# Kernel optimization log

Hardware: AMD Instinct MI355X
Metric: run time of the kernel (lower is better)

Reference implementation:

```python
import jax, jax.numpy as jnp
import numpy as np

N = 50000
E = 800000
FEAT = 128
HID = 128
HEADS = 8
HEAD_DIM = HID // HEADS  # 16
NEG_SLOPE = 0.2


def _gat_layer(x, W, a_src, a_dst, b, src, dst, num_nodes):
    # x: [N, Fin]; W: [Fin, H*C]; a_src/a_dst: [H, C]; b: [H*C]
    H, C = a_src.shape
    h = (x @ W).reshape(num_nodes, H, C)               # [N,H,C]
    alpha_s = jnp.einsum('nhc,hc->nh', h, a_src)       # [N,H]
    alpha_d = jnp.einsum('nhc,hc->nh', h, a_dst)       # [N,H]
    e = jax.nn.leaky_relu(alpha_s[src] + alpha_d[dst], NEG_SLOPE)  # [E,H]
    # segment softmax over destination nodes (every node has a self-loop)
    m = jax.ops.segment_max(e, dst, num_segments=num_nodes)
    e = jnp.exp(e - m[dst])
    s = jax.ops.segment_sum(e, dst, num_segments=num_nodes)
    alpha = e / (s[dst] + 1e-16)                       # [E,H]
    msg = alpha[:, :, None] * h[src]                   # [E,H,C]
    out = jax.ops.segment_sum(msg, dst, num_segments=num_nodes)
    return out.reshape(num_nodes, H * C) + b


def setup_inputs() -> dict:
    key = jax.random.key(0)
    ks = jax.random.split(key, 12)
    x = jax.random.normal(ks[0], (N, FEAT), dtype=jnp.float32)
    edge_index = jax.random.randint(ks[1], (2, E), 0, N, dtype=jnp.int32)
    glorot = lambda k, shape: jax.random.uniform(
        k, shape, jnp.float32,
        -jnp.sqrt(6.0 / (shape[-2] + shape[-1])),
        jnp.sqrt(6.0 / (shape[-2] + shape[-1])))
    W1 = glorot(ks[2], (FEAT, HID))
    a_src1 = glorot(ks[3], (HEADS, HEAD_DIM))
    a_dst1 = glorot(ks[4], (HEADS, HEAD_DIM))
    b1 = jnp.zeros((HID,), jnp.float32)
    W2 = glorot(ks[5], (HID, HID))
    a_src2 = glorot(ks[6], (HEADS, HEAD_DIM))
    a_dst2 = glorot(ks[7], (HEADS, HEAD_DIM))
    b2 = jnp.zeros((HID,), jnp.float32)
    return {"x": x, "edge_index": edge_index,
            "W1": W1, "a_src1": a_src1, "a_dst1": a_dst1, "b1": b1,
            "W2": W2, "a_src2": a_src2, "a_dst2": a_dst2, "b2": b2}


def reference(x, edge_index, W1, a_src1, a_dst1, b1, W2, a_src2, a_dst2, b2):
    # GATConv adds self-loops to the (dense_to_sparse-derived) edge list
    loops = jnp.arange(N, dtype=edge_index.dtype)
    src = jnp.concatenate([edge_index[0], loops])
    dst = jnp.concatenate([edge_index[1], loops])
    h = _gat_layer(x, W1, a_src1, a_dst1, b1, src, dst, N)
    h = jax.nn.elu(h)
    # dropout: inference mode (training=False) -> identity
    h = _gat_layer(h, W2, a_src2, a_dst2, b2, src, dst, N)
    return jax.nn.elu(h)
```

## Files before the change

### kernel.cpp

```cpp
#include <hip/hip_runtime.h>
#include <hip/hip_fp16.h>
#include <math.h>

#define DEGMAX 64
#define CHUNK  2048
#define CAPB   6144

typedef _Float16 half8 __attribute__((ext_vector_type(8)));
typedef float    f32x4 __attribute__((ext_vector_type(4)));

__global__ __launch_bounds__(256) void k_bin(
        const int* __restrict__ src, const int* __restrict__ dst, int E, int K,
        int* __restrict__ gcur, unsigned* __restrict__ bstore) {
    __shared__ int lcnt[256];
    __shared__ int gbase[256];
    int t = threadIdx.x;
    if (t < K) lcnt[t] = 0;
    __syncthreads();
    int e0 = blockIdx.x * CHUNK;
    unsigned pk[8]; short bk[8], rk[8];
    #pragma unroll
    for (int j = 0; j < 8; j++) {
        int e = e0 + t + j * 256;
        bool v = e < E;
        int s = v ? src[e] : 0;
        int d = v ? dst[e] : 0;
        int b = d >> 8;
        pk[j] = ((unsigned)(d & 255) << 16) | (unsigned)s;
        bk[j] = (short)b;
        rk[j] = v ? (short)atomicAdd(&lcnt[b], 1) : (short)-1;
    }
    __syncthreads();
    if (t < K) gbase[t] = lcnt[t] ? atomicAdd(&gcur[t], lcnt[t]) : 0;
    __syncthreads();
    #pragma unroll
    for (int j = 0; j < 8; j++) {
        if (rk[j] >= 0) {
            int b = bk[j];
            int pos = gbase[b] + rk[j];
            if (pos < CAPB) bstore[(size_t)b * CAPB + pos] = pk[j];
        }
    }
}

__global__ __launch_bounds__(256) void k_csr(
        const int* __restrict__ gcur, const unsigned* __restrict__ bstore,
        int N, int* __restrict__ cnt, int* __restrict__ offs,
        unsigned short* __restrict__ adj) {
    int b = blockIdx.x;
    int t = threadIdx.x;
    int n0 = b << 8;
    int nb = N - n0; if (nb > 256) nb = 256;
    int ecnt = gcur[b]; if (ecnt > CAPB) ecnt = CAPB;
    __shared__ int lcnt[256], lofs[256], wsum[4];
    __shared__ unsigned short stage[CAPB];
    const unsigned* bp = bstore + (size_t)b * CAPB;

    lcnt[t] = 0;
    __syncthreads();
    for (int i = t; i < ecnt; i += 256)
        atomicAdd(&lcnt[bp[i] >> 16], 1);
    __syncthreads();
    int mycnt = lcnt[t];
    int lane = t & 63, wv = t >> 6;
    int x = mycnt;
    #pragma unroll
    for (int d = 1; d < 64; d <<= 1) {
        int y = __shfl_up(x, d);
        if (lane >= d) x += y;
    }
    if (lane == 63) wsum[wv] = x;
    __syncthreads();
    int base = 0;
    for (int k = 0; k < wv; k++) base += wsum[k];
    int myofs = base + x - mycnt;
    lofs[t] = myofs;
    if (t < nb) {
        cnt[n0 + t]  = mycnt;
        offs[n0 + t] = b * CAPB + myofs;
    }
    __syncthreads();
    lcnt[t] = 0;
    __syncthreads();
    for (int i = t; i < ecnt; i += 256) {
        unsigned p = bp[i];
        int node = p >> 16;
        int r = atomicAdd(&lcnt[node], 1);
        stage[lofs[node] + r] = (unsigned short)(p & 0xffffu);
    }
    __syncthreads();
    for (int i = t; i < ecnt; i += 256)
        adj[(size_t)b * CAPB + i] = stage[i];
}

__global__ void k_wcast(const float* __restrict__ W, __half* __restrict__ Wfrag) {
    int id = blockIdx.x * blockDim.x + threadIdx.x;
    if (id >= 2048) return;
    int lane = id & 63;
    int ct = (id >> 6) & 7;
    int kc = id >> 9;
    int q = lane >> 4, n = lane & 15;
    #pragma unroll
    for (int j = 0; j < 8; j++) {
        int k = kc * 32 + q * 8 + j;
        int c = ct * 16 + n;
        Wfrag[(size_t)id * 8 + j] = __float2half(W[(size_t)k * 128 + c]);
    }
}

__device__ inline float4 ld4f(const float* p) { return *(const float4*)p; }

template<typename InT>
__global__ __launch_bounds__(256) void k_gemm_mfma(
        const InT* __restrict__ X, const __half* __restrict__ Wfrag,
        const float* __restrict__ a_src, const float* __restrict__ a_dst,
        __half* __restrict__ H16, float* __restrict__ as_out,
        float* __restrict__ ad_out, int M) {
    __shared__ __half xls[64][136];
    int t = threadIdx.x;
    int w = t >> 6, lane = t & 63;
    int q = lane >> 4, n = lane & 15;
    int row0 = blockIdx.x * 64;

    half8 bfrag[4][2];
    #pragma unroll
    for (int kc = 0; kc < 4; kc++)
        #pragma unroll
        for (int c2 = 0; c2 < 2; c2++) {
            int ct = w * 2 + c2;
            uint4 u = *(const uint4*)(Wfrag + (((size_t)(kc * 8 + ct)) * 64 + lane) * 8);
            bfrag[kc][c2] = *(half8*)&u;
        }

    #pragma unroll
    for (int rep = 0; rep < 8; rep++) {
        int lin = rep * 1024 + t * 4;
        int r = lin >> 7, k = lin & 127;
        int gr = row0 + r;
        uint2 u;
        if constexpr (sizeof(InT) == 4) {
            float4 v = (gr < M) ? ld4f((const float*)&X[(size_t)gr * 128 + k])
                                : make_float4(0.f, 0.f, 0.f, 0.f);
            __half2 h0 = __floats2half2_rn(v.x, v.y);
            __half2 h1 = __floats2half2_rn(v.z, v.w);
            u = make_uint2(*(unsigned*)&h0, *(unsigned*)&h1);
        } else {
            u = (gr < M) ? *(const uint2*)&X[(size_t)gr * 128 + k] : make_uint2(0, 0);
        }
        *(uint2*)&xls[r][k] = u;
    }
    __syncthreads();

    f32x4 acc[4][2];
    #pragma unroll
    for (int rt = 0; rt < 4; rt++)
        #pragma unroll
        for (int c2 = 0; c2 < 2; c2++)
            acc[rt][c2] = (f32x4){0.f, 0.f, 0.f, 0.f};

    #pragma unroll
    for (int kc = 0; kc < 4; kc++)
        #pragma unroll
        for (int rt = 0; rt < 4; rt++) {
            uint4 au = *(const uint4*)&xls[rt * 16 + n][kc * 32 + q * 8];
            half8 af = *(half8*)&au;
            acc[rt][0] = __builtin_amdgcn_mfma_f32_16x16x32_f16(af, bfrag[kc][0], acc[rt][0], 0, 0, 0);
            acc[rt][1] = __builtin_amdgcn_mfma_f32_16x16x32_f16(af, bfrag[kc][1], acc[rt][1], 0, 0, 0);
        }

    #pragma unroll
    for (int c2 = 0; c2 < 2; c2++) {
        int h = w * 2 + c2;
        float avs = a_src[h * 16 + n];
        float avd = a_dst[h * 16 + n];
        #pragma unroll
        for (int rt = 0; rt < 4; rt++)
            #pragma unroll
            for (int reg = 0; reg < 4; reg++) {
                int grow = row0 + rt * 16 + q * 4 + reg;
                float val = acc[rt][c2][reg];
                if (grow < M) H16[(size_t)grow * 128 + h * 16 + n] = __float2half(val);
                float ps = val * avs, pd = val * avd;
                ps += __shfl_xor(ps, 1); ps += __shfl_xor(ps, 2);
                ps += __shfl_xor(ps, 4); ps += __shfl_xor(ps, 8);
                pd += __shfl_xor(pd, 1); pd += __shfl_xor(pd, 2);
                pd += __shfl_xor(pd, 4); pd += __shfl_xor(pd, 8);
                if (n == 0 && grow < M) {
                    as_out[grow * 8 + h] = ps;
                    ad_out[grow * 8 + h] = pd;
                }
            }
    }
}

#define LOADB(ii, LG, HR)                                                     \
    {                                                                         \
        int e_ = (ii) + (lane >> 3);                                          \
        int se_ = __shfl(sv, (e_ < deg) ? e_ : 0);                            \
        LG = as_[(size_t)se_ * 8 + (lane & 7)];                               \
        _Pragma("unroll")                                                     \
        for (int j_ = 0; j_ < 8; j_++) {                                      \
            int idx_ = (ii) + j_; if (idx_ >= deg) idx_ = deg - 1;            \
            int sj_ = __shfl(sv, idx_);                                       \
            HR[j_] = *(const unsigned*)&H[(size_t)sj_ * 128 + lane * 2];      \
        }                                                                     \
    }

template<typename OutT>
__global__ __launch_bounds__(256) void k_aggregate(
        const __half* __restrict__ H, const float* __restrict__ as_,
        const float* __restrict__ ad_, const int* __restrict__ cnt,
        const int* __restrict__ offs, const unsigned short* __restrict__ adj,
        const float* __restrict__ bias, OutT* __restrict__ out, int N) {
    int wave = (int)((blockIdx.x * blockDim.x + threadIdx.x) >> 6);
    int lane = threadIdx.x & 63;
    if (wave >= N) return;
    int n = wave;
    int hd = lane >> 3;
    int deg = cnt[n]; if (deg > DEGMAX) deg = DEGMAX;
    int row = offs[n];
    int sv = (lane < deg) ? (int)adj[row + lane] : n;
    float adv = ad_[n * 8 + (lane & 7)];

    float vs = as_[n * 8 + hd] + ad_[n * 8 + hd];
    vs = vs > 0.f ? vs : 0.2f * vs;
    float wsf = __expf(vs);
    unsigned hrs = *(const unsigned*)&H[(size_t)n * 128 + lane * 2];
    float2 hvs = __half22float2(*(__half2*)&hrs);
    float ssum = wsf, ax = wsf * hvs.x, ay = wsf * hvs.y;

    float lgt_c; unsigned hraw_c[8];
    if (deg > 0) LOADB(0, lgt_c, hraw_c);
    for (int i = 0; i < deg; i += 8) {
        float lgt_n; unsigned hraw_n[8];
        int inext = i + 8;
        if (inext < deg) LOADB(inext, lgt_n, hraw_n);
        float v = lgt_c + adv;
        v = v > 0.f ? v : 0.2f * v;
        float wgt = (i + (lane >> 3) < deg) ? __expf(v) : 0.f;
        #pragma unroll
        for (int j = 0; j < 8; j++) {
            float wj = __shfl(wgt, j * 8 + hd);
            float2 hv = __half22float2(*(__half2*)&hraw_c[j]);
            ssum += wj; ax += wj * hv.x; ay += wj * hv.y;
        }
        lgt_c = lgt_n;
        #pragma unroll
        for (int j = 0; j < 8; j++) hraw_c[j] = hraw_n[j];
    }
    float inv = 1.f / (ssum + 1e-16f);
    float ox = ax * inv + bias[lane * 2];
    float oy = ay * inv + bias[lane * 2 + 1];
    ox = ox > 0.f ? ox : __expf(ox) - 1.f;
    oy = oy > 0.f ? oy : __expf(oy) - 1.f;
    if constexpr (sizeof(OutT) == 2) {
        __half2 hv = __floats2half2_rn(ox, oy);
        *(__half2*)&out[(size_t)n * 128 + lane * 2] = hv;
    } else {
        *(float2*)&out[(size_t)n * 128 + lane * 2] = make_float2(ox, oy);
    }
}

static inline char* bump(char*& w, size_t bytes) {
    char* p = w;
    w += (bytes + 255) & ~(size_t)255;
    return p;
}

extern "C" void kernel_launch(void* const* d_in, const int* in_sizes, int n_in,
                              void* d_out, int out_size, void* d_ws, size_t ws_size,
                              hipStream_t stream) {
    const float* x   = (const float*)d_in[0];
    const int*   ei  = (const int*)d_in[1];
    const float* W1  = (const float*)d_in[2];
    const float* as1 = (const float*)d_in[3];
    const float* ad1 = (const float*)d_in[4];
    const float* b1  = (const float*)d_in[5];
    const float* W2  = (const float*)d_in[6];
    const float* as2 = (const float*)d_in[7];
    const float* ad2 = (const float*)d_in[8];
    const float* b2  = (const float*)d_in[9];
    float* out = (float*)d_out;

    int N = in_sizes[0] / 128;
    int E = in_sizes[1] / 2;
    const int* srcs = ei;
    const int* dsts = ei + E;
    int K = (N + 255) >> 8;

    char* w = (char*)d_ws;
    int*            cnt   = (int*)           bump(w, (size_t)N * sizeof(int));
    int*            offs  = (int*)           bump(w, (size_t)N * sizeof(int));
    int*            gcur  = (int*)           bump(w, 256 * sizeof(int));
    unsigned*       bst   = (unsigned*)      bump(w, (size_t)256 * CAPB * sizeof(unsigned));
    unsigned short* adj   = (unsigned short*)bump(w, (size_t)256 * CAPB * sizeof(unsigned short));
    __half*         H16   = (__half*)        bump(w, (size_t)N * 128 * sizeof(__half));
    __half*         A16   = (__half*)        bump(w, (size_t)N * 128 * sizeof(__half));
    float*          asb   = (float*)         bump(w, (size_t)N * 8 * sizeof(float));
    float*          adb   = (float*)         bump(w, (size_t)N * 8 * sizeof(float));
    __half*         Wf1   = (__half*)        bump(w, 16384 * sizeof(__half));
    __half*         Wf2   = (__half*)        bump(w, 16384 * sizeof(__half));

    hipMemsetAsync(gcur, 0, 256 * sizeof(int), stream);
    k_wcast<<<8, 256, 0, stream>>>(W1, Wf1);
    k_wcast<<<8, 256, 0, stream>>>(W2, Wf2);
    k_bin<<<(E + CHUNK - 1) / CHUNK, 256, 0, stream>>>(srcs, dsts, E, K, gcur, bst);
    k_csr<<<K, 256, 0, stream>>>(gcur, bst, N, cnt, offs, adj);

    k_gemm_mfma<float><<<(N + 63) / 64, 256, 0, stream>>>(x, Wf1, as1, ad1, H16, asb, adb, N);
    k_aggregate<__half><<<(N + 3) / 4, 256, 0, stream>>>(H16, asb, adb, cnt, offs, adj, b1, A16, N);

    k_gemm_mfma<__half><<<(N + 63) / 64, 256, 0, stream>>>(A16, Wf2, as2, ad2, H16, asb, adb, N);
    k_aggregate<float><<<(N + 3) / 4, 256, 0, stream>>>(H16, asb, adb, cnt, offs, adj, b2, out, N);
}
```

Before: 234.4 us.

## Batch first 32 neighbor loads in aggregate and merge setup launches

The aggregation kernel now issues gathers for up to four 8-edge batches (32 neighbors) before doing any compute, in place of a one-batch-ahead double buffer. This exposes more memory-level parallelism per wave for the typical degree of about 17. Edges past 32 fall back to a plain load-then-compute loop with no prefetch. Separately, the two weight-cast launches and the memset of the bin cursor are merged into one kernel, removing two launch overheads; the four register batches raise register pressure and may lower occupancy.

```diff
diff --git a/kernel.cpp b/kernel.cpp
--- a/kernel.cpp
+++ b/kernel.cpp
@@ -93,9 +93,15 @@
         adj[(size_t)b * CAPB + i] = stage[i];
 }
 
-__global__ void k_wcast(const float* __restrict__ W, __half* __restrict__ Wfrag) {
-    int id = blockIdx.x * blockDim.x + threadIdx.x;
-    if (id >= 2048) return;
+__global__ void k_wcast(const float* __restrict__ W1, __half* __restrict__ Wf1,
+                        const float* __restrict__ W2, __half* __restrict__ Wf2,
+                        int* __restrict__ gcur) {
+    int t = threadIdx.x;
+    if (blockIdx.x == 0) gcur[t] = 0;
+    int id2 = blockIdx.x * blockDim.x + t;
+    const float* W = (id2 < 2048) ? W1 : W2;
+    __half* Wf = (id2 < 2048) ? Wf1 : Wf2;
+    int id = id2 & 2047;
     int lane = id & 63;
     int ct = (id >> 6) & 7;
     int kc = id >> 9;
@@ -104,7 +110,7 @@
     for (int j = 0; j < 8; j++) {
         int k = kc * 32 + q * 8 + j;
         int c = ct * 16 + n;
-        Wfrag[(size_t)id * 8 + j] = __float2half(W[(size_t)k * 128 + c]);
+        Wf[(size_t)id * 8 + j] = __float2half(W[(size_t)k * 128 + c]);
     }
 }
 
@@ -206,6 +212,19 @@
         }                                                                     \
     }
 
+#define COMPB(ii, LG, HR)                                                     \
+    {                                                                         \
+        float v_ = LG + adv;                                                  \
+        v_ = v_ > 0.f ? v_ : 0.2f * v_;                                       \
+        float wgt_ = ((ii) + (lane >> 3) < deg) ? __expf(v_) : 0.f;           \
+        _Pragma("unroll")                                                     \
+        for (int j_ = 0; j_ < 8; j_++) {                                      \
+            float wj_ = __shfl(wgt_, j_ * 8 + hd);                            \
+            float2 hv_ = __half22float2(*(__half2*)&HR[j_]);                  \
+            ssum += wj_; ax += wj_ * hv_.x; ay += wj_ * hv_.y;                \
+        }                                                                     \
+    }
+
 template<typename OutT>
 __global__ __launch_bounds__(256) void k_aggregate(
         const __half* __restrict__ H, const float* __restrict__ as_,
@@ -229,25 +248,22 @@
     float2 hvs = __half22float2(*(__half2*)&hrs);
     float ssum = wsf, ax = wsf * hvs.x, ay = wsf * hvs.y;
 
-    float lgt_c; unsigned hraw_c[8];
-    if (deg > 0) LOADB(0, lgt_c, hraw_c);
-    for (int i = 0; i < deg; i += 8) {
-        float lgt_n; unsigned hraw_n[8];
-        int inext = i + 8;
-        if (inext < deg) LOADB(inext, lgt_n, hraw_n);
-        float v = lgt_c + adv;
-        v = v > 0.f ? v : 0.2f * v;
-        float wgt = (i + (lane >> 3) < deg) ? __expf(v) : 0.f;
-        #pragma unroll
-        for (int j = 0; j < 8; j++) {
-            float wj = __shfl(wgt, j * 8 + hd);
-            float2 hv = __half22float2(*(__half2*)&hraw_c[j]);
-            ssum += wj; ax += wj * hv.x; ay += wj * hv.y;
-        }
-        lgt_c = lgt_n;
-        #pragma unroll
-        for (int j = 0; j < 8; j++) hraw_c[j] = hraw_n[j];
-    }
+    float lg0, lg1, lg2, lg3;
+    unsigned hr0[8], hr1[8], hr2[8], hr3[8];
+    if (deg > 0)  LOADB(0,  lg0, hr0);
+    if (deg > 8)  LOADB(8,  lg1, hr1);
+    if (deg > 16) LOADB(16, lg2, hr2);
+    if (deg > 24) LOADB(24, lg3, hr3);
+    if (deg > 0)  COMPB(0,  lg0, hr0);
+    if (deg > 8)  COMPB(8,  lg1, hr1);
+    if (deg > 16) COMPB(16, lg2, hr2);
+    if (deg > 24) COMPB(24, lg3, hr3);
+    for (int i = 32; i < deg; i += 8) {
+        float lgt; unsigned hrt[8];
+        LOADB(i, lgt, hrt);
+        COMPB(i, lgt, hrt);
+    }
+
     float inv = 1.f / (ssum + 1e-16f);
     float ox = ax * inv + bias[lane * 2];
     float oy = ay * inv + bias[lane * 2 + 1];
@@ -301,9 +317,7 @@
     __half*         Wf1   = (__half*)        bump(w, 16384 * sizeof(__half));
     __half*         Wf2   = (__half*)        bump(w, 16384 * sizeof(__half));
 
-    hipMemsetAsync(gcur, 0, 256 * sizeof(int), stream);
-    k_wcast<<<8, 256, 0, stream>>>(W1, Wf1);
-    k_wcast<<<8, 256, 0, stream>>>(W2, Wf2);
+    k_wcast<<<16, 256, 0, stream>>>(W1, Wf1, W2, Wf2, gcur);
     k_bin<<<(E + CHUNK - 1) / CHUNK, 256, 0, stream>>>(srcs, dsts, E, K, gcur, bst);
     k_csr<<<K, 256, 0, stream>>>(gcur, bst, N, cnt, offs, adj);
 
```

Result: faster. 229.5 us (-2.1%).
